# Kernel tuning notes

Hardware: AMD Instinct MI355X
Metric: run time of the kernel (lower is better)

Reference implementation:

```python
import jax, jax.numpy as jnp
import numpy as np


def setup_inputs() -> dict:
    key = jax.random.key(0)
    ks = jax.random.split(key, 12)
    B, IN, H = 4096, 512, 1024
    s = lambda k, shape, scale: jax.random.normal(k, shape, dtype=jnp.float32) * scale
    inp = {
        "inputs": s(ks[0], (B, IN), 1.0),
        "h0": s(ks[1], (B, H), 1.0),
        "c0": s(ks[2], (B, H), 1.0),
        "ts": jax.random.uniform(ks[3], (B, 2), dtype=jnp.float32),
        "w_ih": s(ks[4], (4 * H, IN), 1.0 / np.sqrt(IN)),
        "w_hh": s(ks[5], (4 * H, H), 1.0 / np.sqrt(H)),
        "b_ih": s(ks[6], (4 * H,), 1.0 / np.sqrt(H)),
        "b_hh": s(ks[7], (4 * H,), 1.0 / np.sqrt(H)),
        "w1": s(ks[8], (H, H), 1.0 / np.sqrt(H)),
        "b1": s(ks[9], (H,), 1.0 / np.sqrt(H)),
        "w2": s(ks[10], (H, H), 1.0 / np.sqrt(H)),
        "b2": s(ks[11], (H,), 1.0 / np.sqrt(H)),
    }
    return inp


def _lstm_cell(x, h, c, w_ih, w_hh, b_ih, b_hh):
    # gates: [B, 4H] in PyTorch (i, f, g, o) order
    gates = x @ w_ih.T + h @ w_hh.T + b_ih + b_hh
    i, f, g, o = jnp.split(gates, 4, axis=-1)
    i, f, o = jax.nn.sigmoid(i), jax.nn.sigmoid(f), jax.nn.sigmoid(o)
    g = jnp.tanh(g)
    c_new = f * c + i * g
    h_new = o * jnp.tanh(c_new)
    return h_new, c_new


def reference(inputs, h0, c0, ts, w_ih, w_hh, b_ih, b_hh, w1, b1, w2, b2):
    # Two stacked LSTMCell applications sharing the same weights
    h, c = _lstm_cell(inputs, h0, c0, w_ih, w_hh, b_ih, b_hh)
    h, c = _lstm_cell(inputs, h, c, w_ih, w_hh, b_ih, b_hh)

    # Autonomous ODE func: Linear -> Tanh -> Linear
    f = lambda y: jnp.tanh(y @ w1.T + b1) @ w2.T + b2

    # One RK4 step per sample from ts[:,0] to ts[:,1] (batched, no python loop)
    dt = (ts[:, 1] - ts[:, 0])[:, None]  # [B, 1]
    k1 = f(h)
    k2 = f(h + 0.5 * dt * k1)
    k3 = f(h + 0.5 * dt * k2)
    k4 = f(h + dt * k3)
    ht = h + (dt / 6.0) * (k1 + 2.0 * k2 + 2.0 * k3 + k4)
    return (ht, c)
```

## Files before the change

kernel.cpp:

```cpp
#include <hip/hip_runtime.h>

typedef short short8 __attribute__((ext_vector_type(8)));
typedef float f32x4 __attribute__((ext_vector_type(4)));
typedef unsigned short u16x8 __attribute__((ext_vector_type(8)));
typedef unsigned short u16x4 __attribute__((ext_vector_type(4)));

#define B_DIM 4096
#define IN_DIM 512
#define H_DIM 1024
#define KCAT 1536

__device__ __forceinline__ float bs2f(unsigned short s) {
    return __uint_as_float(((unsigned int)s) << 16);
}
__device__ __forceinline__ unsigned short f2bs(float f) {
    unsigned int u = __float_as_uint(f);
    u += 0x7fff + ((u >> 16) & 1);
    return (unsigned short)(u >> 16);
}
__device__ __forceinline__ float sigm(float x) { return 1.0f / (1.0f + __expf(-x)); }
__device__ __forceinline__ float ftanh(float x) { return 1.0f - 2.0f / (__expf(2.0f * x) + 1.0f); }

__device__ __forceinline__ int gperm(int r) {
    int g = r >> 10, j = r & 1023;
    return ((j >> 4) << 6) + (g << 4) + (j & 15);
}

#define T0 262144
#define T1 786432
#define T2 1048576
#define T3 1572864
#define T4 1703936
#define T5 1835008
__device__ __forceinline__ u16x8 cvt8(const float* __restrict__ in, long i) {
    float4 a = *(const float4*)(in + i);
    float4 b = *(const float4*)(in + i + 4);
    u16x8 o;
    o[0] = f2bs(a.x); o[1] = f2bs(a.y); o[2] = f2bs(a.z); o[3] = f2bs(a.w);
    o[4] = f2bs(b.x); o[5] = f2bs(b.y); o[6] = f2bs(b.z); o[7] = f2bs(b.w);
    return o;
}
__global__ __launch_bounds__(256) void pack_all(const float* __restrict__ x,
                                                const float* __restrict__ h0,
                                                const float* __restrict__ wih,
                                                const float* __restrict__ whh,
                                                const float* __restrict__ w1,
                                                const float* __restrict__ w2,
                                                unsigned short* __restrict__ xb,
                                                unsigned short* __restrict__ hb0,
                                                unsigned short* __restrict__ wcat,
                                                unsigned short* __restrict__ w116,
                                                unsigned short* __restrict__ w216) {
    long g = (long)blockIdx.x * 256 + threadIdx.x;
    if (g < T0) {
        long i = g * 8;
        *(u16x8*)(xb + i) = cvt8(x, i);
    } else if (g < T1) {
        long i = (g - T0) * 8;
        *(u16x8*)(hb0 + i) = cvt8(h0, i);
    } else if (g < T2) {
        long i = (g - T1) * 8;
        int r = (int)(i / IN_DIM), c = (int)(i % IN_DIM);
        *(u16x8*)(wcat + (size_t)gperm(r) * KCAT + c) = cvt8(wih, i);
    } else if (g < T3) {
        long i = (g - T2) * 8;
        int r = (int)(i / H_DIM), c = (int)(i % H_DIM);
        *(u16x8*)(wcat + (size_t)gperm(r) * KCAT + IN_DIM + c) = cvt8(whh, i);
    } else if (g < T4) {
        long i = (g - T3) * 8;
        *(u16x8*)(w116 + i) = cvt8(w1, i);
    } else if (g < T5) {
        long i = (g - T4) * 8;
        *(u16x8*)(w216 + i) = cvt8(w2, i);
    }
}

__global__ __launch_bounds__(256) void transp_w2(const float* __restrict__ w2,
                                                 unsigned short* __restrict__ w2t) {
    int tid = blockIdx.x * 256 + threadIdx.x;
    int t = tid & 1023;
    int jb = tid >> 10;
    float4 a = *(const float4*)(w2 + (size_t)t * H_DIM + jb * 8);
    float4 b = *(const float4*)(w2 + (size_t)t * H_DIM + jb * 8 + 4);
    float v[8] = {a.x, a.y, a.z, a.w, b.x, b.y, b.z, b.w};
    #pragma unroll
    for (int q = 0; q < 8; ++q)
        w2t[(size_t)(jb * 8 + q) * H_DIM + t] = f2bs(v[q]);
}

__global__ __launch_bounds__(256) void bck(const float* __restrict__ b2,
                                           const float* __restrict__ w1,
                                           float* __restrict__ bc) {
    __shared__ float ws[4];
    int n = blockIdx.x;
    int t = threadIdx.x;
    float4 bv = *(const float4*)(b2 + t * 4);
    float4 wv = *(const float4*)(w1 + (size_t)n * H_DIM + t * 4);
    float p = bv.x * wv.x + bv.y * wv.y + bv.z * wv.z + bv.w * wv.w;
    #pragma unroll
    for (int off = 32; off > 0; off >>= 1) p += __shfl_down(p, off);
    if ((t & 63) == 0) ws[t >> 6] = p;
    __syncthreads();
    if (t == 0) bc[n] = ws[0] + ws[1] + ws[2] + ws[3];
}

__global__ __launch_bounds__(256) void prep_small(const float* __restrict__ bih,
                                                  const float* __restrict__ bhh,
                                                  const float* __restrict__ ts,
                                                  float* __restrict__ bsum,
                                                  float* __restrict__ dtv,
                                                  int n4h, int nb) {
    int i = blockIdx.x * blockDim.x + threadIdx.x;
    if (i < n4h) bsum[gperm(i)] = bih[i] + bhh[i];
    if (i < nb)  dtv[i] = ts[2 * i + 1] - ts[2 * i];
}

template <int MODE>
__global__ __launch_bounds__(512) void gemm8(
    const unsigned short* __restrict__ A,
    const unsigned short* __restrict__ W,
    const float* __restrict__ bias,
    unsigned short* __restrict__ gx,
    unsigned short* __restrict__ h_out,
    float* __restrict__ c_out,
    const float* __restrict__ c_in) {
    constexpr int KA = (MODE == 0) ? IN_DIM : H_DIM;
    constexpr int NT = KA / 32;
    __shared__ unsigned short lA[3][128 * 32];
    __shared__ unsigned short lB[3][256 * 32];
    const int t = threadIdx.x;
    const int lane = t & 63;
    const int wave = t >> 6;
    const int wm = (wave >> 2) * 64;
    const int wn = (wave & 3) * 64;
    const int fr = lane & 15;
    const int kb = lane >> 4;
    const int tile_m = blockIdx.y * 128;
    const int tile_n = blockIdx.x * 256;

    f32x4 acc[4][4];
    #pragma unroll
    for (int i = 0; i < 4; ++i)
        #pragma unroll
        for (int j = 0; j < 4; ++j)
            acc[i][j] = (f32x4){0.f, 0.f, 0.f, 0.f};

    int aoff[4], boff[4];
    #pragma unroll
    for (int i = 0; i < 4; ++i) {
        int arow = wm + i * 16 + fr;
        aoff[i] = arow * 32 + (kb ^ ((arow >> 1) & 3)) * 8;
    }
    #pragma unroll
    for (int j = 0; j < 4; ++j) {
        int brow = wn + j * 16 + fr;
        boff[j] = brow * 32 + (kb ^ ((brow >> 1) & 3)) * 8;
    }

    auto stageA = [&](int kt) {
        const int buf = kt % 3;
        int row = t >> 2;
        int g = t & 3;
        int gs = g ^ ((row >> 1) & 3);
        int kk = kt * 32 + gs * 8;
        __builtin_amdgcn_global_load_lds(
            (__attribute__((address_space(1))) void*)(A + (size_t)(tile_m + row) * KA + kk),
            (__attribute__((address_space(3))) void*)(&lA[buf][row * 32 + g * 8]), 16, 0, 0);
    };
    auto stageB = [&](int kt) {
        const int buf = kt % 3;
        #pragma unroll
        for (int j = 0; j < 2; ++j) {
            int idx = j * 512 + t;
            int row = idx >> 2;
            int g = idx & 3;
            int gs = g ^ ((row >> 1) & 3);
            int kk = kt * 32 + gs * 8;
            __builtin_amdgcn_global_load_lds(
                (__attribute__((address_space(1))) void*)(W + (size_t)(tile_n + row) * KCAT + kk),
                (__attribute__((address_space(3))) void*)(&lB[buf][row * 32 + g * 8]), 16, 0, 0);
        }
    };

    stageA(0); stageB(0);
    stageA(1); stageB(1);

    for (int kt = 0; kt < NT; ++kt) {
        const int buf = kt % 3;
        if (kt + 1 < NT) asm volatile("s_waitcnt vmcnt(3)" ::: "memory");
        else             asm volatile("s_waitcnt vmcnt(0)" ::: "memory");
        __builtin_amdgcn_s_barrier();
        asm volatile("" ::: "memory");
        short8 bfr[4], af[4];
        #pragma unroll
        for (int j = 0; j < 4; ++j) bfr[j] = *(const short8*)&lB[buf][boff[j]];
        #pragma unroll
        for (int i = 0; i < 4; ++i) af[i] = *(const short8*)&lA[buf][aoff[i]];
        __builtin_amdgcn_s_setprio(1);
        #pragma unroll
        for (int i = 0; i < 4; ++i)
            #pragma unroll
            for (int j = 0; j < 4; ++j)
                acc[i][j] = __builtin_amdgcn_mfma_f32_16x16x32_bf16(af[i], bfr[j], acc[i][j], 0, 0, 0);
        __builtin_amdgcn_s_setprio(0);
        if (kt + 2 < NT) { stageA(kt + 2); stageB(kt + 2); }
        asm volatile("" ::: "memory");
    }

    const int jbase = ((tile_n + wn) >> 6) << 4;
    if (MODE == 0) {
        float bv[4];
        #pragma unroll
        for (int g = 0; g < 4; ++g) bv[g] = bias[tile_n + wn + g * 16 + fr];
        #pragma unroll
        for (int i = 0; i < 4; ++i) {
            #pragma unroll
            for (int r = 0; r < 4; ++r) {
                const int m = tile_m + wm + i * 16 + kb * 4 + r;
                const int j = jbase + fr;
                u16x4 o;
                #pragma unroll
                for (int g = 0; g < 4; ++g) o[g] = f2bs(acc[i][g][r] + bv[g]);
                *(u16x4*)(gx + ((size_t)m * H_DIM + j) * 4) = o;
            }
        }
    } else {
        #pragma unroll
        for (int i = 0; i < 4; ++i) {
            #pragma unroll
            for (int r = 0; r < 4; ++r) {
                const int m = tile_m + wm + i * 16 + kb * 4 + r;
                const int j = jbase + fr;
                u16x4 gv = *(const u16x4*)(gx + ((size_t)m * H_DIM + j) * 4);
                float ig = sigm(acc[i][0][r] + bs2f(gv[0]));
                float fg = sigm(acc[i][1][r] + bs2f(gv[1]));
                float gg = ftanh(acc[i][2][r] + bs2f(gv[2]));
                float og = sigm(acc[i][3][r] + bs2f(gv[3]));
                float cin = c_in[(size_t)m * H_DIM + j];
                float cn = fg * cin + ig * gg;
                float hn = og * ftanh(cn);
                h_out[(size_t)m * H_DIM + j] = f2bs(hn);
                c_out[(size_t)m * H_DIM + j] = cn;
            }
        }
    }
}

template <int EPI>
__global__ __launch_bounds__(256) void gemm2(
    const unsigned short* __restrict__ A1,
    const unsigned short* __restrict__ W,
    const int M, const int N, const int K,
    const float* __restrict__ bias,
    unsigned short* __restrict__ outb,
    float* __restrict__ outf,
    const float* __restrict__ z1f,
    float* __restrict__ Uf,
    const unsigned short* __restrict__ hmat,
    const float* __restrict__ dtv,
    const float alpha, const float cw, const int first, const int last) {
    constexpr int BM = 64, BN = 64, BK = 64;
    constexpr int MR = 2, NR = 2;
    __shared__ unsigned short lA[2][BM * BK];
    __shared__ unsigned short lB[2][BN * BK];
    const int t = threadIdx.x;
    const int lane = t & 63;
    const int wave = t >> 6;
    const int wm = (wave >> 1) * 32;
    const int wn = (wave & 1) * 32;
    const int fr = lane & 15;
    const int kb = lane >> 4;
    const int tile_m = blockIdx.y * BM;
    const int tile_n = blockIdx.x * BN;

    f32x4 acc[MR][NR];
    #pragma unroll
    for (int i = 0; i < MR; ++i)
        #pragma unroll
        for (int j = 0; j < NR; ++j)
            acc[i][j] = (f32x4){0.f, 0.f, 0.f, 0.f};

    const unsigned short* aptr1 = A1 + (size_t)tile_m * K;
    const unsigned short* wptr  = W + (size_t)tile_n * K;

    auto stage = [&](int kt) {
        const int buf = kt & 1;
        const int k0 = kt * BK;
        #pragma unroll
        for (int j = 0; j < 2; ++j) {
            int idx = j * 256 + t;
            int row = idx >> 3;
            int g = idx & 7;
            int col = (g ^ (row & 7)) * 8;
            __builtin_amdgcn_global_load_lds(
                (__attribute__((address_space(1))) void*)(aptr1 + (size_t)row * K + k0 + col),
                (__attribute__((address_space(3))) void*)(&lA[buf][row * BK + g * 8]), 16, 0, 0);
        }
        #pragma unroll
        for (int j = 0; j < 2; ++j) {
            int idx = j * 256 + t;
            int row = idx >> 3;
            int g = idx & 7;
            int col = (g ^ (row & 7)) * 8;
            __builtin_amdgcn_global_load_lds(
                (__attribute__((address_space(1))) void*)(wptr + (size_t)row * K + k0 + col),
                (__attribute__((address_space(3))) void*)(&lB[buf][row * BK + g * 8]), 16, 0, 0);
        }
    };

    const int NT = K / BK;
    stage(0);
    for (int kt = 0; kt < NT; ++kt) {
        const int buf = kt & 1;
        asm volatile("s_waitcnt vmcnt(0)" ::: "memory");
        __builtin_amdgcn_s_barrier();
        asm volatile("" ::: "memory");
        short8 af[2][MR], bfr[2][NR];
        #pragma unroll
        for (int h = 0; h < 2; ++h) {
            #pragma unroll
            for (int i = 0; i < MR; ++i) {
                int arow = wm + i * 16 + fr;
                int gidx = h * 4 + kb;
                af[h][i] = *(const short8*)&lA[buf][arow * BK + (gidx ^ (arow & 7)) * 8];
            }
            #pragma unroll
            for (int j = 0; j < NR; ++j) {
                int brow = wn + j * 16 + fr;
                int gidx = h * 4 + kb;
                bfr[h][j] = *(const short8*)&lB[buf][brow * BK + (gidx ^ (brow & 7)) * 8];
            }
        }
        if (kt + 1 < NT) stage(kt + 1);
        #pragma unroll
        for (int h = 0; h < 2; ++h)
            #pragma unroll
            for (int i = 0; i < MR; ++i)
                #pragma unroll
                for (int j = 0; j < NR; ++j)
                    acc[i][j] = __builtin_amdgcn_mfma_f32_16x16x32_bf16(af[h][i], bfr[h][j], acc[i][j], 0, 0, 0);
        asm volatile("" ::: "memory");
    }

    #pragma unroll
    for (int i = 0; i < MR; ++i) {
        #pragma unroll
        for (int r = 0; r < 4; ++r) {
            const int m = tile_m + wm + i * 16 + kb * 4 + r;
            float dt = 0.f;
            if (EPI >= 6) dt = dtv[m];
            #pragma unroll
            for (int j = 0; j < NR; ++j) {
                const int n = tile_n + wn + j * 16 + fr;
                const size_t off = (size_t)m * N + n;
                float v = acc[i][j][r];
                if (EPI == 0) {
                    if (bias) v += bias[n];
                    outb[off] = f2bs(v);
                } else if (EPI == 5) {
                    v += bias[n];
                    outf[off] = v;
                    outb[off] = f2bs(ftanh(v));
                } else if (EPI == 6) {
                    v += bias[n];
                    float z1v = z1f[off];
                    float z = z1v + alpha * dt * v;
                    float u = ftanh(z);
                    if (first) {
                        Uf[off] = ftanh(z1v) + cw * u;
                        outb[off] = f2bs(u);
                    } else if (last) {
                        outb[off] = f2bs(Uf[off] + cw * u);
                    } else {
                        Uf[off] = Uf[off] + cw * u;
                        outb[off] = f2bs(u);
                    }
                } else {
                    float hv = bs2f(hmat[off]);
                    outf[off] = hv + dt * (v * (1.0f / 6.0f) + bias[n]);
                }
            }
        }
    }
}

extern "C" void kernel_launch(void* const* d_in, const int* in_sizes, int n_in,
                              void* d_out, int out_size, void* d_ws, size_t ws_size,
                              hipStream_t stream) {
    int IX = 0, IH0 = 1, IC0 = 2, ITS = 3, IWIH = 4, IWHH = 5, IBIH = 6, IBHH = 7,
        IW1 = 8, IB1 = 9, IW2 = 10, IB2 = 11;
    const bool sorted_ok = n_in >= 12 &&
        in_sizes[0] == 1024 && in_sizes[1] == 1024 && in_sizes[2] == 4096 &&
        in_sizes[3] == 4096 && in_sizes[4] == 4194304 && in_sizes[5] == 4194304 &&
        in_sizes[6] == 2097152 && in_sizes[7] == 8192 && in_sizes[8] == 1048576 &&
        in_sizes[9] == 1048576 && in_sizes[10] == 4194304 && in_sizes[11] == 2097152;
    if (sorted_ok) {
        IB1 = 0; IB2 = 1; IBHH = 2; IBIH = 3; IC0 = 4; IH0 = 5;
        IX = 6; ITS = 7; IW1 = 8; IW2 = 9; IWHH = 10; IWIH = 11;
    }
    const float* x_f   = (const float*)d_in[IX];
    const float* h0_f  = (const float*)d_in[IH0];
    const float* c0_f  = (const float*)d_in[IC0];
    const float* ts_f  = (const float*)d_in[ITS];
    const float* wih_f = (const float*)d_in[IWIH];
    const float* whh_f = (const float*)d_in[IWHH];
    const float* bih_f = (const float*)d_in[IBIH];
    const float* bhh_f = (const float*)d_in[IBHH];
    const float* w1_f  = (const float*)d_in[IW1];
    const float* b1_f  = (const float*)d_in[IB1];
    const float* w2_f  = (const float*)d_in[IW2];
    const float* b2_f  = (const float*)d_in[IB2];

    constexpr size_t SZ_BIN  = (size_t)B_DIM * IN_DIM;
    constexpr size_t SZ_BH   = (size_t)B_DIM * H_DIM;
    constexpr size_t SZ_HH   = (size_t)H_DIM * H_DIM;
    constexpr size_t SZ_WCAT = (size_t)4 * H_DIM * KCAT;

    float* bsum = (float*)d_ws;
    float* dtv  = bsum + 4 * H_DIM;
    float* bc   = dtv + B_DIM;
    float* S    = bc + H_DIM;
    float* c1f  = S + SZ_BH;
    unsigned short* wcat = (unsigned short*)(c1f + SZ_BH);
    unsigned short* w116 = wcat + SZ_WCAT;
    unsigned short* w216 = w116 + SZ_HH;
    unsigned short* w2t  = w216 + SZ_HH;
    unsigned short* wc16 = w2t + SZ_HH;
    unsigned short* xb   = wc16 + SZ_HH;
    unsigned short* hb0  = xb + SZ_BIN;
    unsigned short* hb1  = hb0 + SZ_BH;
    unsigned short* hb2  = hb1 + SZ_BH;
    unsigned short* ubuf = hb2 + SZ_BH;
    unsigned short* ybuf = ubuf + SZ_BH;
    unsigned short* Gx   = ybuf + SZ_BH;

    float* out_ht = (float*)d_out;
    float* out_c  = out_ht + SZ_BH;
    float* z1f = S;
    float* Uf  = c1f;

    const int TB = 256;
    pack_all<<<T5 / TB, TB, 0, stream>>>(x_f, h0_f, wih_f, whh_f, w1_f, w2_f,
                                         xb, hb0, wcat, w116, w216);
    transp_w2<<<(H_DIM * H_DIM / 8) / TB, TB, 0, stream>>>(w2_f, w2t);
    prep_small<<<(4 * H_DIM) / TB, TB, 0, stream>>>(bih_f, bhh_f, ts_f, bsum, dtv, 4 * H_DIM, B_DIM);
    bck<<<H_DIM, TB, 0, stream>>>(b2_f, w1_f, bc);

    dim3 g8(4 * H_DIM / 256, B_DIM / 128);
    dim3 gSm(H_DIM / 64, B_DIM / 64);
    dim3 gWc(H_DIM / 64, H_DIM / 64);

    gemm2<0><<<gWc, TB, 0, stream>>>(w116, w2t, H_DIM, H_DIM, H_DIM, nullptr,
                                     wc16, nullptr, nullptr, nullptr, nullptr, nullptr, 0.f, 0.f, 0, 0);

    gemm8<0><<<g8, 512, 0, stream>>>(xb, wcat, bsum, Gx, nullptr, nullptr, nullptr);

    gemm8<1><<<g8, 512, 0, stream>>>(hb0, wcat + IN_DIM, nullptr, Gx, hb1, S, c0_f);
    gemm8<1><<<g8, 512, 0, stream>>>(hb1, wcat + IN_DIM, nullptr, Gx, hb2, out_c, S);

    gemm2<5><<<gSm, TB, 0, stream>>>(hb2, w116, B_DIM, H_DIM, H_DIM, b1_f,
                                     ubuf, z1f, nullptr, nullptr, nullptr, nullptr, 0.f, 0.f, 0, 0);
    gemm2<6><<<gSm, TB, 0, stream>>>(ubuf, wc16, B_DIM, H_DIM, H_DIM, bc,
                                     ybuf, nullptr, z1f, Uf, nullptr, dtv, 0.5f, 2.0f, 1, 0);
    gemm2<6><<<gSm, TB, 0, stream>>>(ybuf, wc16, B_DIM, H_DIM, H_DIM, bc,
                                     ubuf, nullptr, z1f, Uf, nullptr, dtv, 0.5f, 2.0f, 0, 0);
    gemm2<6><<<gSm, TB, 0, stream>>>(ubuf, wc16, B_DIM, H_DIM, H_DIM, bc,
                                     hb1, nullptr, z1f, Uf, nullptr, dtv, 1.0f, 1.0f, 0, 1);
    gemm2<7><<<gSm, TB, 0, stream>>>(hb1, w216, B_DIM, H_DIM, H_DIM, b2_f,
                                     nullptr, out_ht, nullptr, nullptr, hb2, dtv, 0.f, 0.f, 0, 0);
}
```

Before: 274.9 us.

## Prefetch next k-tile LDS fragments into registers to overlap with MFMA

Both GEMM kernels now double-buffer the register fragments: the next k-tile's A/B fragments are read from LDS before the current tile's MFMAs run, hiding LDS read latency. gemm2 moves from two to three LDS stages with a prefetch distance of two and precomputes the swizzled LDS offsets. However, the wait changes to vmcnt(0) inside the loop, which waits for all outstanding global loads, including the just-issued kt+2 stage, and so may serialise the global prefetch. It also costs more registers and LDS.

```diff
diff --git a/kernel.cpp b/kernel.cpp
--- a/kernel.cpp
+++ b/kernel.cpp
@@ -184,27 +184,37 @@
 
     stageA(0); stageB(0);
     stageA(1); stageB(1);
+    asm volatile("s_waitcnt vmcnt(3)" ::: "memory");
+    __builtin_amdgcn_s_barrier();
+    asm volatile("" ::: "memory");
+    short8 afc[4], bfc[4], afn[4], bfn[4];
+    #pragma unroll
+    for (int j = 0; j < 4; ++j) bfc[j] = *(const short8*)&lB[0][boff[j]];
+    #pragma unroll
+    for (int i = 0; i < 4; ++i) afc[i] = *(const short8*)&lA[0][aoff[i]];
 
     for (int kt = 0; kt < NT; ++kt) {
-        const int buf = kt % 3;
-        if (kt + 1 < NT) asm volatile("s_waitcnt vmcnt(3)" ::: "memory");
-        else             asm volatile("s_waitcnt vmcnt(0)" ::: "memory");
-        __builtin_amdgcn_s_barrier();
-        asm volatile("" ::: "memory");
-        short8 bfr[4], af[4];
-        #pragma unroll
-        for (int j = 0; j < 4; ++j) bfr[j] = *(const short8*)&lB[buf][boff[j]];
-        #pragma unroll
-        for (int i = 0; i < 4; ++i) af[i] = *(const short8*)&lA[buf][aoff[i]];
+        if (kt + 1 < NT) {
+            asm volatile("s_waitcnt vmcnt(0)" ::: "memory");
+            __builtin_amdgcn_s_barrier();
+            asm volatile("" ::: "memory");
+            const int nbuf = (kt + 1) % 3;
+            #pragma unroll
+            for (int j = 0; j < 4; ++j) bfn[j] = *(const short8*)&lB[nbuf][boff[j]];
+            #pragma unroll
+            for (int i = 0; i < 4; ++i) afn[i] = *(const short8*)&lA[nbuf][aoff[i]];
+        }
         __builtin_amdgcn_s_setprio(1);
         #pragma unroll
         for (int i = 0; i < 4; ++i)
             #pragma unroll
             for (int j = 0; j < 4; ++j)
-                acc[i][j] = __builtin_amdgcn_mfma_f32_16x16x32_bf16(af[i], bfr[j], acc[i][j], 0, 0, 0);
+                acc[i][j] = __builtin_amdgcn_mfma_f32_16x16x32_bf16(afc[i], bfc[j], acc[i][j], 0, 0, 0);
         __builtin_amdgcn_s_setprio(0);
         if (kt + 2 < NT) { stageA(kt + 2); stageB(kt + 2); }
         asm volatile("" ::: "memory");
+        #pragma unroll
+        for (int i = 0; i < 4; ++i) { afc[i] = afn[i]; bfc[i] = bfn[i]; }
     }
 
     const int jbase = ((tile_n + wn) >> 6) << 4;
@@ -261,8 +271,8 @@
     const float alpha, const float cw, const int first, const int last) {
     constexpr int BM = 64, BN = 64, BK = 64;
     constexpr int MR = 2, NR = 2;
-    __shared__ unsigned short lA[2][BM * BK];
-    __shared__ unsigned short lB[2][BN * BK];
+    __shared__ unsigned short lA[3][BM * BK];
+    __shared__ unsigned short lB[3][BN * BK];
     const int t = threadIdx.x;
     const int lane = t & 63;
     const int wave = t >> 6;
@@ -280,11 +290,26 @@
         for (int j = 0; j < NR; ++j)
             acc[i][j] = (f32x4){0.f, 0.f, 0.f, 0.f};
 
+    int aoffs[2][MR], boffs[2][NR];
+    #pragma unroll
+    for (int h = 0; h < 2; ++h) {
+        #pragma unroll
+        for (int i = 0; i < MR; ++i) {
+            int arow = wm + i * 16 + fr;
+            aoffs[h][i] = arow * BK + ((h * 4 + kb) ^ (arow & 7)) * 8;
+        }
+        #pragma unroll
+        for (int j = 0; j < NR; ++j) {
+            int brow = wn + j * 16 + fr;
+            boffs[h][j] = brow * BK + ((h * 4 + kb) ^ (brow & 7)) * 8;
+        }
+    }
+
     const unsigned short* aptr1 = A1 + (size_t)tile_m * K;
     const unsigned short* wptr  = W + (size_t)tile_n * K;
 
     auto stage = [&](int kt) {
-        const int buf = kt & 1;
+        const int buf = kt % 3;
         const int k0 = kt * BK;
         #pragma unroll
         for (int j = 0; j < 2; ++j) {
@@ -309,37 +334,49 @@
     };
 
     const int NT = K / BK;
-    stage(0);
+    stage(0); stage(1);
+    asm volatile("s_waitcnt vmcnt(4)" ::: "memory");
+    __builtin_amdgcn_s_barrier();
+    asm volatile("" ::: "memory");
+    short8 afc[2][MR], bfc[2][NR], afn[2][MR], bfn[2][NR];
+    #pragma unroll
+    for (int h = 0; h < 2; ++h) {
+        #pragma unroll
+        for (int i = 0; i < MR; ++i) afc[h][i] = *(const short8*)&lA[0][aoffs[h][i]];
+        #pragma unroll
+        for (int j = 0; j < NR; ++j) bfc[h][j] = *(const short8*)&lB[0][boffs[h][j]];
+    }
+
     for (int kt = 0; kt < NT; ++kt) {
-        const int buf = kt & 1;
-        asm volatile("s_waitcnt vmcnt(0)" ::: "memory");
-        __builtin_amdgcn_s_barrier();
-        asm volatile("" ::: "memory");
-        short8 af[2][MR], bfr[2][NR];
-        #pragma unroll
-        for (int h = 0; h < 2; ++h) {
-            #pragma unroll
-            for (int i = 0; i < MR; ++i) {
-                int arow = wm + i * 16 + fr;
-                int gidx = h * 4 + kb;
-                af[h][i] = *(const short8*)&lA[buf][arow * BK + (gidx ^ (arow & 7)) * 8];
+        if (kt + 1 < NT) {
+            asm volatile("s_waitcnt vmcnt(0)" ::: "memory");
+            __builtin_amdgcn_s_barrier();
+            asm volatile("" ::: "memory");
+            const int nbuf = (kt + 1) % 3;
+            #pragma unroll
+            for (int h = 0; h < 2; ++h) {
+                #pragma unroll
+                for (int i = 0; i < MR; ++i) afn[h][i] = *(const short8*)&lA[nbuf][aoffs[h][i]];
+                #pragma unroll
+                for (int j = 0; j < NR; ++j) bfn[h][j] = *(const short8*)&lB[nbuf][boffs[h][j]];
             }
-            #pragma unroll
-            for (int j = 0; j < NR; ++j) {
-                int brow = wn + j * 16 + fr;
-                int gidx = h * 4 + kb;
-                bfr[h][j] = *(const short8*)&lB[buf][brow * BK + (gidx ^ (brow & 7)) * 8];
-            }
-        }
-        if (kt + 1 < NT) stage(kt + 1);
+        }
         #pragma unroll
         for (int h = 0; h < 2; ++h)
             #pragma unroll
             for (int i = 0; i < MR; ++i)
                 #pragma unroll
                 for (int j = 0; j < NR; ++j)
-                    acc[i][j] = __builtin_amdgcn_mfma_f32_16x16x32_bf16(af[h][i], bfr[h][j], acc[i][j], 0, 0, 0);
+                    acc[i][j] = __builtin_amdgcn_mfma_f32_16x16x32_bf16(afc[h][i], bfc[h][j], acc[i][j], 0, 0, 0);
+        if (kt + 2 < NT) stage(kt + 2);
         asm volatile("" ::: "memory");
+        #pragma unroll
+        for (int h = 0; h < 2; ++h) {
+            #pragma unroll
+            for (int i = 0; i < MR; ++i) afc[h][i] = afn[h][i];
+            #pragma unroll
+            for (int j = 0; j < NR; ++j) bfc[h][j] = bfn[h][j];
+        }
     }
 
     #pragma unroll
```

New measurement: 360.2 us. 31.0% more time.

## Fuse input-projection GEMM into first LSTM cell GEMM over concatenated K

Applied to the files above, without the earlier changes.

The separate x@W_ih GEMM and the first recurrent h0@W_hh GEMM are merged into one kernel that runs over the concatenated K=1536 dimension, reading A from x for the first 512 columns and from h0 for the rest. Partway through the K loop the accumulator plus bias is written out as the bf16 Gx buffer that the second cell reuses, and the LSTM epilogue then runs on the full sum. This saves one kernel launch and the write-then-read of Gx for the first cell, at the cost of a mid-loop store that can stall the pipeline.

```diff
diff --git a/kernel.cpp b/kernel.cpp
--- a/kernel.cpp
+++ b/kernel.cpp
@@ -117,14 +117,15 @@
 
 template <int MODE>
 __global__ __launch_bounds__(512) void gemm8(
-    const unsigned short* __restrict__ A,
+    const unsigned short* __restrict__ A0,
+    const unsigned short* __restrict__ A1,
     const unsigned short* __restrict__ W,
     const float* __restrict__ bias,
     unsigned short* __restrict__ gx,
     unsigned short* __restrict__ h_out,
     float* __restrict__ c_out,
     const float* __restrict__ c_in) {
-    constexpr int KA = (MODE == 0) ? IN_DIM : H_DIM;
+    constexpr int KA = (MODE == 2) ? KCAT : H_DIM;
     constexpr int NT = KA / 32;
     __shared__ unsigned short lA[3][128 * 32];
     __shared__ unsigned short lB[3][256 * 32];
@@ -157,14 +158,28 @@
         boff[j] = brow * 32 + (kb ^ ((brow >> 1) & 3)) * 8;
     }
 
+    float bvs[4] = {0.f, 0.f, 0.f, 0.f};
+    if constexpr (MODE == 2) {
+        #pragma unroll
+        for (int g = 0; g < 4; ++g) bvs[g] = bias[tile_n + wn + g * 16 + fr];
+    }
+    const int jbase = ((tile_n + wn) >> 6) << 4;
+
     auto stageA = [&](int kt) {
         const int buf = kt % 3;
         int row = t >> 2;
         int g = t & 3;
         int gs = g ^ ((row >> 1) & 3);
         int kk = kt * 32 + gs * 8;
+        const unsigned short* src;
+        if constexpr (MODE == 2) {
+            src = (kk < IN_DIM) ? A0 + (size_t)(tile_m + row) * IN_DIM + kk
+                                : A1 + (size_t)(tile_m + row) * H_DIM + (kk - IN_DIM);
+        } else {
+            src = A1 + (size_t)(tile_m + row) * H_DIM + kk;
+        }
         __builtin_amdgcn_global_load_lds(
-            (__attribute__((address_space(1))) void*)(A + (size_t)(tile_m + row) * KA + kk),
+            (__attribute__((address_space(1))) void*)src,
             (__attribute__((address_space(3))) void*)(&lA[buf][row * 32 + g * 8]), 16, 0, 0);
     };
     auto stageB = [&](int kt) {
@@ -203,45 +218,50 @@
             for (int j = 0; j < 4; ++j)
                 acc[i][j] = __builtin_amdgcn_mfma_f32_16x16x32_bf16(af[i], bfr[j], acc[i][j], 0, 0, 0);
         __builtin_amdgcn_s_setprio(0);
+        if constexpr (MODE == 2) {
+            if (kt == (IN_DIM / 32) - 1) {
+                #pragma unroll
+                for (int i = 0; i < 4; ++i) {
+                    #pragma unroll
+                    for (int r = 0; r < 4; ++r) {
+                        const int m = tile_m + wm + i * 16 + kb * 4 + r;
+                        const int j = jbase + fr;
+                        u16x4 o;
+                        #pragma unroll
+                        for (int g = 0; g < 4; ++g) o[g] = f2bs(acc[i][g][r] + bvs[g]);
+                        *(u16x4*)(gx + ((size_t)m * H_DIM + j) * 4) = o;
+                    }
+                }
+            }
+        }
         if (kt + 2 < NT) { stageA(kt + 2); stageB(kt + 2); }
         asm volatile("" ::: "memory");
     }
 
-    const int jbase = ((tile_n + wn) >> 6) << 4;
-    if (MODE == 0) {
-        float bv[4];
-        #pragma unroll
-        for (int g = 0; g < 4; ++g) bv[g] = bias[tile_n + wn + g * 16 + fr];
-        #pragma unroll
-        for (int i = 0; i < 4; ++i) {
-            #pragma unroll
-            for (int r = 0; r < 4; ++r) {
-                const int m = tile_m + wm + i * 16 + kb * 4 + r;
-                const int j = jbase + fr;
-                u16x4 o;
+    #pragma unroll
+    for (int i = 0; i < 4; ++i) {
+        #pragma unroll
+        for (int r = 0; r < 4; ++r) {
+            const int m = tile_m + wm + i * 16 + kb * 4 + r;
+            const int j = jbase + fr;
+            float vg[4];
+            if constexpr (MODE == 2) {
                 #pragma unroll
-                for (int g = 0; g < 4; ++g) o[g] = f2bs(acc[i][g][r] + bv[g]);
-                *(u16x4*)(gx + ((size_t)m * H_DIM + j) * 4) = o;
+                for (int g = 0; g < 4; ++g) vg[g] = acc[i][g][r] + bvs[g];
+            } else {
+                u16x4 gv = *(const u16x4*)(gx + ((size_t)m * H_DIM + j) * 4);
+                #pragma unroll
+                for (int g = 0; g < 4; ++g) vg[g] = acc[i][g][r] + bs2f(gv[g]);
             }
-        }
-    } else {
-        #pragma unroll
-        for (int i = 0; i < 4; ++i) {
-            #pragma unroll
-            for (int r = 0; r < 4; ++r) {
-                const int m = tile_m + wm + i * 16 + kb * 4 + r;
-                const int j = jbase + fr;
-                u16x4 gv = *(const u16x4*)(gx + ((size_t)m * H_DIM + j) * 4);
-                float ig = sigm(acc[i][0][r] + bs2f(gv[0]));
-                float fg = sigm(acc[i][1][r] + bs2f(gv[1]));
-                float gg = ftanh(acc[i][2][r] + bs2f(gv[2]));
-                float og = sigm(acc[i][3][r] + bs2f(gv[3]));
-                float cin = c_in[(size_t)m * H_DIM + j];
-                float cn = fg * cin + ig * gg;
-                float hn = og * ftanh(cn);
-                h_out[(size_t)m * H_DIM + j] = f2bs(hn);
-                c_out[(size_t)m * H_DIM + j] = cn;
-            }
+            float ig = sigm(vg[0]);
+            float fg = sigm(vg[1]);
+            float gg = ftanh(vg[2]);
+            float og = sigm(vg[3]);
+            float cin = c_in[(size_t)m * H_DIM + j];
+            float cn = fg * cin + ig * gg;
+            float hn = og * ftanh(cn);
+            h_out[(size_t)m * H_DIM + j] = f2bs(hn);
+            c_out[(size_t)m * H_DIM + j] = cn;
         }
     }
 }
@@ -453,10 +473,8 @@
     gemm2<0><<<gWc, TB, 0, stream>>>(w116, w2t, H_DIM, H_DIM, H_DIM, nullptr,
                                      wc16, nullptr, nullptr, nullptr, nullptr, nullptr, 0.f, 0.f, 0, 0);
 
-    gemm8<0><<<g8, 512, 0, stream>>>(xb, wcat, bsum, Gx, nullptr, nullptr, nullptr);
-
-    gemm8<1><<<g8, 512, 0, stream>>>(hb0, wcat + IN_DIM, nullptr, Gx, hb1, S, c0_f);
-    gemm8<1><<<g8, 512, 0, stream>>>(hb1, wcat + IN_DIM, nullptr, Gx, hb2, out_c, S);
+    gemm8<2><<<g8, 512, 0, stream>>>(xb, hb0, wcat, bsum, Gx, hb1, S, c0_f);
+    gemm8<1><<<g8, 512, 0, stream>>>(nullptr, hb1, wcat + IN_DIM, nullptr, Gx, hb2, out_c, S);
 
     gemm2<5><<<gSm, TB, 0, stream>>>(hb2, w116, B_DIM, H_DIM, H_DIM, b1_f,
                                      ubuf, z1f, nullptr, nullptr, nullptr, nullptr, 0.f, 0.f, 0, 0);
```

New measurement: 284.7 us. 3.6% more time.
